# Kernel tuning notes

Measured on AMD Instinct MI355X. Metric: run time of the kernel, lower is better.

Reference implementation:

```python
import jax, jax.numpy as jnp
import numpy as np

EPS = 1e-5

def setup_inputs() -> dict:
    key = jax.random.key(0)
    k1, k2 = jax.random.split(key)
    N, D = 8192, 256
    q_features = jax.random.normal(k1, (N, D), dtype=jnp.float32)
    g_features = jax.random.normal(k2, (N, D), dtype=jnp.float32)
    return {"q_features": q_features, "g_features": g_features}

def reference(q_features, g_features):
    # logits[i, j] = q_i . g_j ; original computes row i as g_features @ q_i
    logits = jnp.einsum('id,jd->ij', q_features, g_features)  # [N, N]
    # exp(l_ii)/sum_j exp(l_ij) == softmax row diagonal (stable form, same math)
    probs_diag = jnp.diagonal(jax.nn.softmax(logits, axis=-1))  # [N]
    loss = jnp.mean(-jnp.log(probs_diag + EPS))
    return loss
```

## Files before the change

kernel.cpp:

```cpp
#include <hip/hip_runtime.h>
#include <stdint.h>


#define LOG2E 1.44269504f
#define KOFF  92.3324826f

typedef __attribute__((ext_vector_type(8))) short short8;
typedef __attribute__((ext_vector_type(4))) float f32x4;

typedef __attribute__((address_space(1))) const uint32_t gu32;
typedef __attribute__((address_space(3))) uint32_t lu32;

__device__ __forceinline__ uint32_t pack2bf(float lo, float hi) {
    return __builtin_amdgcn_perm(__float_as_uint(hi), __float_as_uint(lo), 0x07060302u);
}

__global__ __launch_bounds__(256) void k_cvt(const float* __restrict__ q,
                                             const float* __restrict__ g,
                                             uint4* __restrict__ qb,
                                             uint4* __restrict__ gb) {
    int o = blockIdx.x * 256 + threadIdx.x;
    const float* src = q;
    uint4* dst = qb;
    if (o >= 262144) { o -= 262144; src = g; dst = gb; }
    int p   = o >> 11;
    int b   = (o >> 6) & 31;
    int l   = o & 63;
    int row = p * 64 + (b & 3) * 16 + (l & 15);
    int k0  = (b >> 2) * 32 + (l >> 4) * 8;
    const float4* s = (const float4*)(src + row * 256 + k0);
    float4 a = s[0], c = s[1];
    uint4 ov;
    ov.x = pack2bf(a.x, a.y); ov.y = pack2bf(a.z, a.w);
    ov.z = pack2bf(c.x, c.y); ov.w = pack2bf(c.z, c.w);
    dst[o] = ov;
}

__global__ __launch_bounds__(256, 2) void k_main(const uint4* __restrict__ qb,
                                                 const uint4* __restrict__ gb,
                                                 float* __restrict__ zpart,
                                                 float* __restrict__ diag) {
    __shared__ uint4 lds4[2048];
    char* lds = (char*)lds4;
    const int tid  = threadIdx.x;
    const int wave = tid >> 6;
    const int lane = tid & 63;
    const int l15  = lane & 15;
    const int quad = lane >> 4;
    const int t    = blockIdx.x >> 4;
    const int cs   = blockIdx.x & 15;
    const int rowbase = t * 256 + wave * 64;

    short8 afrag[4][8];
    {
        const char* qp = (const char*)qb + (size_t)(t * 4 + wave) * 32768 + (lane << 4);
#pragma unroll
        for (int rg = 0; rg < 4; ++rg)
#pragma unroll
            for (int ks = 0; ks < 8; ++ks)
                afrag[rg][ks] = *(const short8*)(qp + ((ks * 4 + rg) << 10));
    }

    float zacc[4][4];
#pragma unroll
    for (int rg = 0; rg < 4; ++rg)
#pragma unroll
        for (int r = 0; r < 4; ++r) zacc[rg][r] = 0.f;

    const bool bd = (cs == (t >> 1));

    for (int jt = 0; jt < 8; ++jt) {
        const char* gp = (const char*)gb + (size_t)(cs * 8 + jt) * 32768;
        {
            const int off = wave * 8192;
#pragma unroll
            for (int i = 0; i < 8; ++i)
                __builtin_amdgcn_global_load_lds(
                    (gu32*)(gp + off + i * 1024 + (lane << 4)),
                    (lu32*)(lds + off + i * 1024), 16, 0, 0);
        }
        __syncthreads();

        f32x4 acc[4][4];
#pragma unroll
        for (int rg = 0; rg < 4; ++rg)
#pragma unroll
            for (int cf = 0; cf < 4; ++cf) acc[rg][cf] = (f32x4){0.f, 0.f, 0.f, 0.f};

#pragma unroll
        for (int ks = 0; ks < 8; ++ks)
#pragma unroll
            for (int cf = 0; cf < 4; ++cf) {
                short8 b = *(const short8*)(lds + ((ks * 4 + cf) << 10) + (lane << 4));
#pragma unroll
                for (int rg = 0; rg < 4; ++rg)
                    acc[rg][cf] = __builtin_amdgcn_mfma_f32_16x16x32_bf16(
                        afrag[rg][ks], b, acc[rg][cf], 0, 0, 0);
            }

#pragma unroll
        for (int rg = 0; rg < 4; ++rg)
#pragma unroll
            for (int r = 0; r < 4; ++r) {
                float e0 = __builtin_amdgcn_exp2f(fmaf(acc[rg][0][r], LOG2E, -KOFF));
                float e1 = __builtin_amdgcn_exp2f(fmaf(acc[rg][1][r], LOG2E, -KOFF));
                float e2 = __builtin_amdgcn_exp2f(fmaf(acc[rg][2][r], LOG2E, -KOFF));
                float e3 = __builtin_amdgcn_exp2f(fmaf(acc[rg][3][r], LOG2E, -KOFF));
                zacc[rg][r] += (e0 + e1) + (e2 + e3);
            }

        if (bd && ((jt >> 2) == (t & 1))) {
#pragma unroll
            for (int rg = 0; rg < 4; ++rg)
#pragma unroll
                for (int cf = 0; cf < 4; ++cf)
#pragma unroll
                    for (int r = 0; r < 4; ++r) {
                        int rowg = rowbase + rg * 16 + quad * 4 + r;
                        int colg = (cs << 9) + jt * 64 + cf * 16 + l15;
                        if (rowg == colg) diag[rowg] = acc[rg][cf][r];
                    }
        }
        __syncthreads();
    }

#pragma unroll
    for (int d = 1; d < 16; d <<= 1)
#pragma unroll
        for (int rg = 0; rg < 4; ++rg)
#pragma unroll
            for (int r = 0; r < 4; ++r)
                zacc[rg][r] += __shfl_xor(zacc[rg][r], d, 64);

    if (l15 == 0) {
#pragma unroll
        for (int rg = 0; rg < 4; ++rg)
#pragma unroll
            for (int r = 0; r < 4; ++r)
                zpart[(rowbase + rg * 16 + quad * 4 + r) * 16 + cs] = zacc[rg][r];
    }
}

__global__ __launch_bounds__(256) void k_fin1(const float* __restrict__ zpart,
                                              const float* __restrict__ diag,
                                              float* __restrict__ partial) {
    __shared__ float red[4];
    int r = blockIdx.x * 256 + threadIdx.x;
    const float4* z = (const float4*)(zpart + r * 16);
    float4 a = z[0], b = z[1], c = z[2], d = z[3];
    float Z = (((a.x + a.y) + (a.z + a.w)) + ((b.x + b.y) + (b.z + b.w)))
            + (((c.x + c.y) + (c.z + c.w)) + ((d.x + d.y) + (d.z + d.w)));
    float p = __builtin_amdgcn_exp2f(fmaf(diag[r], LOG2E, -KOFF)) / Z;
    float v = -logf(p + 1e-5f);
#pragma unroll
    for (int dd = 1; dd < 64; dd <<= 1) v += __shfl_xor(v, dd, 64);
    if ((threadIdx.x & 63) == 0) red[threadIdx.x >> 6] = v;
    __syncthreads();
    if (threadIdx.x == 0)
        partial[blockIdx.x] = (red[0] + red[1]) + (red[2] + red[3]);
}

__global__ void k_fin2(const float* __restrict__ partial, float* __restrict__ out) {
    float v = (threadIdx.x < 32) ? partial[threadIdx.x] : 0.f;
#pragma unroll
    for (int d = 1; d < 32; d <<= 1) v += __shfl_xor(v, d, 64);
    if (threadIdx.x == 0) out[0] = v * (1.f / 8192.f);
}

extern "C" void kernel_launch(void* const* d_in, const int* in_sizes, int n_in,
                              void* d_out, int out_size, void* d_ws, size_t ws_size,
                              hipStream_t stream) {
    const float* q = (const float*)d_in[0];
    const float* g = (const float*)d_in[1];
    char* ws = (char*)d_ws;
    uint4* qb     = (uint4*)ws;
    uint4* gb     = (uint4*)(ws + (4u << 20));
    float* diag   = (float*)(ws + (8u << 20));
    float* zpart  = (float*)(ws + (8u << 20) + (32u << 10));
    float* partial= (float*)(ws + (8u << 20) + (576u << 10));
    k_cvt <<<2048, 256, 0, stream>>>(q, g, qb, gb);
    k_main<<<512,  256, 0, stream>>>(qb, gb, zpart, diag);
    k_fin1<<<32,   256, 0, stream>>>(zpart, diag, partial);
    k_fin2<<<1,     64, 0, stream>>>(partial, (float*)d_out);
    (void)in_sizes; (void)n_in; (void)out_size; (void)ws_size;
}
```

Before: 105.3 us.

## Load B fragments directly from global and fold log2e scale into conversion

Removes the LDS staging of the g tiles, along with both block-wide barriers per tile. Each wave now reads its B fragments straight from global memory, relying on L1/L2 for reuse across the four waves. Separately, q is pre-multiplied by log2(e) during the bf16 conversion, so the epilogue and the final reduction only subtract the offset instead of doing an fma. Direct global reads add per-wave traffic and latency with no explicit prefetch, and pre-scaling before bf16 rounding slightly changes the precision of the logits.

After: 110.5 us. 1.05x slower.

```diff
diff --git a/kernel.cpp b/kernel.cpp
--- a/kernel.cpp
+++ b/kernel.cpp
@@ -7,9 +7,6 @@
 
 typedef __attribute__((ext_vector_type(8))) short short8;
 typedef __attribute__((ext_vector_type(4))) float f32x4;
-
-typedef __attribute__((address_space(1))) const uint32_t gu32;
-typedef __attribute__((address_space(3))) uint32_t lu32;
 
 __device__ __forceinline__ uint32_t pack2bf(float lo, float hi) {
     return __builtin_amdgcn_perm(__float_as_uint(hi), __float_as_uint(lo), 0x07060302u);
@@ -22,17 +19,18 @@
     int o = blockIdx.x * 256 + threadIdx.x;
     const float* src = q;
     uint4* dst = qb;
-    if (o >= 262144) { o -= 262144; src = g; dst = gb; }
+    float s = LOG2E;
+    if (o >= 262144) { o -= 262144; src = g; dst = gb; s = 1.0f; }
     int p   = o >> 11;
     int b   = (o >> 6) & 31;
     int l   = o & 63;
     int row = p * 64 + (b & 3) * 16 + (l & 15);
     int k0  = (b >> 2) * 32 + (l >> 4) * 8;
-    const float4* s = (const float4*)(src + row * 256 + k0);
-    float4 a = s[0], c = s[1];
+    const float4* sp = (const float4*)(src + row * 256 + k0);
+    float4 a = sp[0], c = sp[1];
     uint4 ov;
-    ov.x = pack2bf(a.x, a.y); ov.y = pack2bf(a.z, a.w);
-    ov.z = pack2bf(c.x, c.y); ov.w = pack2bf(c.z, c.w);
+    ov.x = pack2bf(a.x * s, a.y * s); ov.y = pack2bf(a.z * s, a.w * s);
+    ov.z = pack2bf(c.x * s, c.y * s); ov.w = pack2bf(c.z * s, c.w * s);
     dst[o] = ov;
 }
 
@@ -40,8 +38,6 @@
                                                  const uint4* __restrict__ gb,
                                                  float* __restrict__ zpart,
                                                  float* __restrict__ diag) {
-    __shared__ uint4 lds4[2048];
-    char* lds = (char*)lds4;
     const int tid  = threadIdx.x;
     const int wave = tid >> 6;
     const int lane = tid & 63;
@@ -70,16 +66,7 @@
     const bool bd = (cs == (t >> 1));
 
     for (int jt = 0; jt < 8; ++jt) {
-        const char* gp = (const char*)gb + (size_t)(cs * 8 + jt) * 32768;
-        {
-            const int off = wave * 8192;
-#pragma unroll
-            for (int i = 0; i < 8; ++i)
-                __builtin_amdgcn_global_load_lds(
-                    (gu32*)(gp + off + i * 1024 + (lane << 4)),
-                    (lu32*)(lds + off + i * 1024), 16, 0, 0);
-        }
-        __syncthreads();
+        const char* gp = (const char*)gb + (size_t)(cs * 8 + jt) * 32768 + (lane << 4);
 
         f32x4 acc[4][4];
 #pragma unroll
@@ -91,7 +78,7 @@
         for (int ks = 0; ks < 8; ++ks)
 #pragma unroll
             for (int cf = 0; cf < 4; ++cf) {
-                short8 b = *(const short8*)(lds + ((ks * 4 + cf) << 10) + (lane << 4));
+                short8 b = *(const short8*)(gp + ((ks * 4 + cf) << 10));
 #pragma unroll
                 for (int rg = 0; rg < 4; ++rg)
                     acc[rg][cf] = __builtin_amdgcn_mfma_f32_16x16x32_bf16(
@@ -102,10 +89,10 @@
         for (int rg = 0; rg < 4; ++rg)
 #pragma unroll
             for (int r = 0; r < 4; ++r) {
-                float e0 = __builtin_amdgcn_exp2f(fmaf(acc[rg][0][r], LOG2E, -KOFF));
-                float e1 = __builtin_amdgcn_exp2f(fmaf(acc[rg][1][r], LOG2E, -KOFF));
-                float e2 = __builtin_amdgcn_exp2f(fmaf(acc[rg][2][r], LOG2E, -KOFF));
-                float e3 = __builtin_amdgcn_exp2f(fmaf(acc[rg][3][r], LOG2E, -KOFF));
+                float e0 = __builtin_amdgcn_exp2f(acc[rg][0][r] - KOFF);
+                float e1 = __builtin_amdgcn_exp2f(acc[rg][1][r] - KOFF);
+                float e2 = __builtin_amdgcn_exp2f(acc[rg][2][r] - KOFF);
+                float e3 = __builtin_amdgcn_exp2f(acc[rg][3][r] - KOFF);
                 zacc[rg][r] += (e0 + e1) + (e2 + e3);
             }
 
@@ -121,7 +108,6 @@
                         if (rowg == colg) diag[rowg] = acc[rg][cf][r];
                     }
         }
-        __syncthreads();
     }
 
 #pragma unroll
@@ -150,7 +136,7 @@
     float4 a = z[0], b = z[1], c = z[2], d = z[3];
     float Z = (((a.x + a.y) + (a.z + a.w)) + ((b.x + b.y) + (b.z + b.w)))
             + (((c.x + c.y) + (c.z + c.w)) + ((d.x + d.y) + (d.z + d.w)));
-    float p = __builtin_amdgcn_exp2f(fmaf(diag[r], LOG2E, -KOFF)) / Z;
+    float p = __builtin_amdgcn_exp2f(diag[r] - KOFF) / Z;
     float v = -logf(p + 1e-5f);
 #pragma unroll
     for (int dd = 1; dd < 64; dd <<= 1) v += __shfl_xor(v, dd, 64);
```
